# Kernel optimization log

Hardware: AMD Instinct MI355X
Metric: run time of the kernel (lower is better)

Reference implementation:

```python
import jax, jax.numpy as jnp
import numpy as np

B, NDOC, L, E = 32, 4, 512, 512
SCALE = np.float32(1.0 / np.sqrt(E))
NEG_INF = np.float32(-1e9)


def setup_inputs() -> dict:
    key = jax.random.key(0)
    k1, k2, k3, k4, k5, k6 = jax.random.split(key, 6)
    return {
        "x1": jax.random.normal(k1, (B, L, E), dtype=jnp.float32),
        "x2": jax.random.normal(k2, (B, NDOC, L, E), dtype=jnp.float32),
        "x1_len": jax.random.randint(k3, (B,), 0, L, dtype=jnp.int64),
        "x2_len": jax.random.randint(k4, (B, NDOC), 0, L, dtype=jnp.int64),
        "fusion_w": jax.random.normal(k5, (2 * E, E), dtype=jnp.float32) * 0.02,
        "fusion_b": jnp.zeros((E,), dtype=jnp.float32),
        "out_w": jax.random.normal(k6, (8 * E, 2 * E), dtype=jnp.float32) * 0.02,
        "out_b": jnp.zeros((2 * E,), dtype=jnp.float32),
    }


def reference(x1, x2, x1_len, x2_len, fusion_w, fusion_b, out_w, out_b):
    # Faithful to torch .repeat(1,4,...): concatenate 4 full copies along batch,
    # so attention row i pairs x1[i % B] with x2[i // 4, i % 4].
    x1_rep = jnp.tile(x1, (NDOC, 1, 1))          # [4B, L, E]
    x2_r = x2.reshape(-1, L, E)                  # [4B, L, E]

    x1_len_r = jnp.tile(x1_len, NDOC)            # [4B] (same tiling as x1_rep)
    x2_len_r = x2_len.reshape(-1)                # [4B]
    pos = jnp.arange(L)
    q_mask = pos[None, :] < x1_len_r[:, None]    # [4B, L]
    k_mask = pos[None, :] < x2_len_r[:, None]    # [4B, L]
    mask = q_mask[:, :, None] & k_mask[:, None, :]  # [4B, L, L]

    # scaled-dot-product attention with masked_fill(mask==0, -1e9)
    scores = jnp.einsum('bqe,bke->bqk', x1_rep, x2_r) * SCALE  # [4B, L, L]
    scores = jnp.where(mask, scores, NEG_INF)
    attn = jax.nn.softmax(scores, axis=-1)
    x1_att = jnp.einsum('bqk,bke->bqe', attn, x2_r)            # [4B, L, E]

    cat = jnp.concatenate([x1_rep - x1_att, x1_rep * x1_att], axis=-1)  # [4B, L, 2E]
    fus = jax.nn.relu(cat @ fusion_w + fusion_b)                        # [4B, L, E]

    x1_mean = jnp.mean(fus, axis=1)              # [4B, E]
    x1_max = jnp.max(fus, axis=1)                # [4B, E]
    pooled = jnp.concatenate([x1_mean.reshape(B, -1), x1_max.reshape(B, -1)], axis=-1)  # [B, 8E]
    out = jax.nn.relu(pooled @ out_w + out_b)    # [B, 2E]
    return out, attn
```

## Files before the change

kernel.cpp:

```cpp
#include <hip/hip_runtime.h>
#include <cstddef>

#define BATCH 32
#define NB    128
#define LL    512
#define EE    512
#define SCALE 0.044194173824159216f
#define NEG_INF -1e9f

typedef __attribute__((ext_vector_type(4))) float f32x4;
typedef __attribute__((ext_vector_type(8))) short s16x8;
typedef __attribute__((ext_vector_type(4))) unsigned short u16x4;

__device__ __forceinline__ unsigned short f2b(float f) {
    unsigned u = __float_as_uint(f);
    u += 0x7FFFu + ((u >> 16) & 1u);
    return (unsigned short)(u >> 16);
}
__device__ __forceinline__ float b2f(unsigned short h) {
    return __uint_as_float(((unsigned)h) << 16);
}

__global__ __launch_bounds__(256) void k_cvt_x1(
    const float* __restrict__ x1, unsigned short* __restrict__ x1bf)
{
    const size_t idx = (size_t)blockIdx.x * 256 + threadIdx.x;
    f32x4 v = *(const f32x4*)(x1 + idx * 4);
    u16x4 o = { f2b(v[0]), f2b(v[1]), f2b(v[2]), f2b(v[3]) };
    *(u16x4*)(x1bf + idx * 4) = o;
}

__global__ __launch_bounds__(256) void k_cvt_x2(
    const float* __restrict__ x2,
    unsigned short* __restrict__ x2bf, unsigned short* __restrict__ x2t)
{
    __shared__ float T[64][65];
    const int i = blockIdx.z, kb = blockIdx.y * 64, eb = blockIdx.x * 64;
    const float* src = x2 + (size_t)i * LL * EE;
    unsigned short* db = x2bf + (size_t)i * LL * EE;
    unsigned short* dt = x2t  + (size_t)i * LL * EE;
    const int t = threadIdx.x, r16 = t >> 4, c4 = (t & 15) * 4;
#pragma unroll
    for (int p = 0; p < 4; ++p) {
        int row = p * 16 + r16;
        f32x4 v = *(const f32x4*)(src + (size_t)(kb + row) * EE + eb + c4);
        T[row][c4] = v[0]; T[row][c4+1] = v[1]; T[row][c4+2] = v[2]; T[row][c4+3] = v[3];
        u16x4 o = { f2b(v[0]), f2b(v[1]), f2b(v[2]), f2b(v[3]) };
        *(u16x4*)(db + (size_t)(kb + row) * EE + eb + c4) = o;
    }
    __syncthreads();
#pragma unroll
    for (int p = 0; p < 4; ++p) {
        int erow = p * 16 + r16;
        u16x4 o = { f2b(T[c4][erow]), f2b(T[c4+1][erow]),
                    f2b(T[c4+2][erow]), f2b(T[c4+3][erow]) };
        *(u16x4*)(dt + (size_t)(eb + erow) * LL + kb + c4) = o;
    }
}

__global__ __launch_bounds__(256) void k_cvt_fw(
    const float* __restrict__ fw, unsigned short* __restrict__ fwt)
{
    __shared__ float T[64][65];
    const int jb = blockIdx.y * 64, eb = blockIdx.x * 64;
    const int t = threadIdx.x, r16 = t >> 4, c4 = (t & 15) * 4;
#pragma unroll
    for (int p = 0; p < 4; ++p) {
        int row = p * 16 + r16;
        f32x4 v = *(const f32x4*)(fw + (size_t)(jb + row) * EE + eb + c4);
        T[row][c4] = v[0]; T[row][c4+1] = v[1]; T[row][c4+2] = v[2]; T[row][c4+3] = v[3];
    }
    __syncthreads();
#pragma unroll
    for (int p = 0; p < 4; ++p) {
        int erow = p * 16 + r16;
        u16x4 o = { f2b(T[c4][erow]), f2b(T[c4+1][erow]),
                    f2b(T[c4+2][erow]), f2b(T[c4+3][erow]) };
        *(u16x4*)(fwt + (size_t)(eb + erow) * 1024 + jb + c4) = o;
    }
}

__global__ __launch_bounds__(256) void k_scores_mfma(
    const unsigned short* __restrict__ x1bf,
    const unsigned short* __restrict__ x2bf,
    const int* __restrict__ x1_len, const int* __restrict__ x2_len,
    float* __restrict__ attn)
{
    __shared__ unsigned short Al[128 * 40];
    __shared__ unsigned short Bl[128 * 40];
    const int i  = blockIdx.x;
    const int q0 = (blockIdx.y >> 2) * 128;
    const int k0 = (blockIdx.y & 3) * 128;
    const unsigned short* Ag = x1bf + (size_t)(i & 31) * LL * EE;
    const unsigned short* Bg = x2bf + (size_t)i * LL * EE;
    const int t = threadIdx.x, lane = t & 63;
    const int w = t >> 6, wrow = w >> 1, wcol = w & 1;
    const int m = lane & 15, quad = lane >> 4;
    const int srow = t >> 1, shalf = (t & 1) * 16;

    f32x4 acc[4][4];
#pragma unroll
    for (int r = 0; r < 4; ++r)
#pragma unroll
        for (int c = 0; c < 4; ++c) acc[r][c] = (f32x4){0.f, 0.f, 0.f, 0.f};

    for (int e0 = 0; e0 < EE; e0 += 32) {
        s16x8 a0 = *(const s16x8*)(Ag + (size_t)(q0 + srow) * EE + e0 + shalf);
        s16x8 a1 = *(const s16x8*)(Ag + (size_t)(q0 + srow) * EE + e0 + shalf + 8);
        s16x8 b0 = *(const s16x8*)(Bg + (size_t)(k0 + srow) * EE + e0 + shalf);
        s16x8 b1 = *(const s16x8*)(Bg + (size_t)(k0 + srow) * EE + e0 + shalf + 8);
        __syncthreads();
        *(s16x8*)&Al[srow * 40 + shalf]     = a0;
        *(s16x8*)&Al[srow * 40 + shalf + 8] = a1;
        *(s16x8*)&Bl[srow * 40 + shalf]     = b0;
        *(s16x8*)&Bl[srow * 40 + shalf + 8] = b1;
        __syncthreads();
        s16x8 af[4], bfr[4];
#pragma unroll
        for (int rt = 0; rt < 4; ++rt)
            af[rt] = *(const s16x8*)&Al[(wrow * 64 + rt * 16 + m) * 40 + quad * 8];
#pragma unroll
        for (int ct = 0; ct < 4; ++ct)
            bfr[ct] = *(const s16x8*)&Bl[(wcol * 64 + ct * 16 + m) * 40 + quad * 8];
#pragma unroll
        for (int rt = 0; rt < 4; ++rt)
#pragma unroll
            for (int ct = 0; ct < 4; ++ct)
                acc[rt][ct] = __builtin_amdgcn_mfma_f32_16x16x32_bf16(
                    af[rt], bfr[ct], acc[rt][ct], 0, 0, 0);
    }

    const int qlen = x1_len[i & 31];
    const int klen = x2_len[i];
    float* op = attn + (size_t)i * LL * LL;
#pragma unroll
    for (int rt = 0; rt < 4; ++rt) {
#pragma unroll
        for (int reg = 0; reg < 4; ++reg) {
            const int q = q0 + wrow * 64 + rt * 16 + quad * 4 + reg;
            const bool qok = q < qlen;
#pragma unroll
            for (int ct = 0; ct < 4; ++ct) {
                const int k = k0 + wcol * 64 + ct * 16 + m;
                float v = (qok && k < klen) ? acc[rt][ct][reg] * SCALE : NEG_INF;
                op[(size_t)q * LL + k] = v;
            }
        }
    }
}

__global__ __launch_bounds__(256) void k_softmax(
    float* __restrict__ attn, unsigned short* __restrict__ attnbf)
{
    const int row  = blockIdx.x * 4 + (threadIdx.x >> 6);
    const int lane = threadIdx.x & 63;
    float* p = attn + (size_t)row * LL + lane * 8;
    float4 v0 = *(float4*)p;
    float4 v1 = *(float4*)(p + 4);
    float mx = fmaxf(fmaxf(fmaxf(v0.x, v0.y), fmaxf(v0.z, v0.w)),
                     fmaxf(fmaxf(v1.x, v1.y), fmaxf(v1.z, v1.w)));
#pragma unroll
    for (int o = 32; o > 0; o >>= 1) mx = fmaxf(mx, __shfl_xor(mx, o));
    v0.x = __expf(v0.x - mx); v0.y = __expf(v0.y - mx);
    v0.z = __expf(v0.z - mx); v0.w = __expf(v0.w - mx);
    v1.x = __expf(v1.x - mx); v1.y = __expf(v1.y - mx);
    v1.z = __expf(v1.z - mx); v1.w = __expf(v1.w - mx);
    float s = v0.x + v0.y + v0.z + v0.w + v1.x + v1.y + v1.z + v1.w;
#pragma unroll
    for (int o = 32; o > 0; o >>= 1) s += __shfl_xor(s, o);
    const float inv = 1.0f / s;
    v0.x *= inv; v0.y *= inv; v0.z *= inv; v0.w *= inv;
    v1.x *= inv; v1.y *= inv; v1.z *= inv; v1.w *= inv;
    *(float4*)p = v0;
    *(float4*)(p + 4) = v1;
    unsigned short* pb = attnbf + (size_t)row * LL + lane * 8;
    u16x4 o0 = { f2b(v0.x), f2b(v0.y), f2b(v0.z), f2b(v0.w) };
    u16x4 o1 = { f2b(v1.x), f2b(v1.y), f2b(v1.z), f2b(v1.w) };
    *(u16x4*)pb       = o0;
    *(u16x4*)(pb + 4) = o1;
}

__global__ __launch_bounds__(256) void k_pv_mfma(
    const unsigned short* __restrict__ attnbf,
    const unsigned short* __restrict__ x2t,
    const unsigned short* __restrict__ x1bf,
    unsigned short* __restrict__ Cbuf)
{
    __shared__ unsigned short Al[128 * 40];
    __shared__ unsigned short Bl[128 * 40];
    const int i  = blockIdx.x;
    const int q0 = (blockIdx.y >> 2) * 128;
    const int e0 = (blockIdx.y & 3) * 128;
    const unsigned short* Ag = attnbf + (size_t)i * LL * LL;
    const unsigned short* Bg = x2t   + (size_t)i * LL * EE;
    const int t = threadIdx.x, lane = t & 63;
    const int w = t >> 6, wrow = w >> 1, wcol = w & 1;
    const int m = lane & 15, quad = lane >> 4;
    const int srow = t >> 1, shalf = (t & 1) * 16;

    f32x4 acc[4][4];
#pragma unroll
    for (int r = 0; r < 4; ++r)
#pragma unroll
        for (int c = 0; c < 4; ++c) acc[r][c] = (f32x4){0.f, 0.f, 0.f, 0.f};

    for (int kk0 = 0; kk0 < LL; kk0 += 32) {
        s16x8 a0 = *(const s16x8*)(Ag + (size_t)(q0 + srow) * LL + kk0 + shalf);
        s16x8 a1 = *(const s16x8*)(Ag + (size_t)(q0 + srow) * LL + kk0 + shalf + 8);
        s16x8 b0 = *(const s16x8*)(Bg + (size_t)(e0 + srow) * LL + kk0 + shalf);
        s16x8 b1 = *(const s16x8*)(Bg + (size_t)(e0 + srow) * LL + kk0 + shalf + 8);
        __syncthreads();
        *(s16x8*)&Al[srow * 40 + shalf]     = a0;
        *(s16x8*)&Al[srow * 40 + shalf + 8] = a1;
        *(s16x8*)&Bl[srow * 40 + shalf]     = b0;
        *(s16x8*)&Bl[srow * 40 + shalf + 8] = b1;
        __syncthreads();
        s16x8 af[4], bfr[4];
#pragma unroll
        for (int rt = 0; rt < 4; ++rt)
            af[rt] = *(const s16x8*)&Al[(wrow * 64 + rt * 16 + m) * 40 + quad * 8];
#pragma unroll
        for (int ct = 0; ct < 4; ++ct)
            bfr[ct] = *(const s16x8*)&Bl[(wcol * 64 + ct * 16 + m) * 40 + quad * 8];
#pragma unroll
        for (int rt = 0; rt < 4; ++rt)
#pragma unroll
            for (int ct = 0; ct < 4; ++ct)
                acc[rt][ct] = __builtin_amdgcn_mfma_f32_16x16x32_bf16(
                    af[rt], bfr[ct], acc[rt][ct], 0, 0, 0);
    }

    const unsigned short* x1p = x1bf + (size_t)(i & 31) * LL * EE;
    unsigned short* Cb = Cbuf + (size_t)i * LL * 1024;
#pragma unroll
    for (int rt = 0; rt < 4; ++rt) {
#pragma unroll
        for (int reg = 0; reg < 4; ++reg) {
            const int l = q0 + wrow * 64 + rt * 16 + quad * 4 + reg;
#pragma unroll
            for (int ct = 0; ct < 4; ++ct) {
                const int e = e0 + wcol * 64 + ct * 16 + m;
                float att = acc[rt][ct][reg];
                float xv  = b2f(x1p[(size_t)l * EE + e]);
                Cb[(size_t)l * 1024 + e]       = f2b(xv - att);
                Cb[(size_t)l * 1024 + 512 + e] = f2b(xv * att);
            }
        }
    }
}

__global__ __launch_bounds__(256) void k_fuse_mfma(
    const unsigned short* __restrict__ Cbuf,
    const unsigned short* __restrict__ fwt,
    const float* __restrict__ fb,
    float* __restrict__ pmean, float* __restrict__ pmax)
{
    __shared__ unsigned short Al[128 * 40];
    __shared__ unsigned short Bl[128 * 40];
    __shared__ float psum[2][128];
    __shared__ float pmx[2][128];
    const int i  = blockIdx.x;
    const int lt = blockIdx.y >> 2;
    const int e0 = (blockIdx.y & 3) * 128;
    const unsigned short* Ab = Cbuf + ((size_t)i * LL + lt * 128) * 1024;
    const int t = threadIdx.x, lane = t & 63;
    const int w = t >> 6, wrow = w >> 1, wcol = w & 1;
    const int m = lane & 15, quad = lane >> 4;
    const int srow = t >> 1, shalf = (t & 1) * 16;

    float bias[4];
#pragma unroll
    for (int ct = 0; ct < 4; ++ct) bias[ct] = fb[e0 + wcol * 64 + ct * 16 + m];
    float csum[4] = {0.f, 0.f, 0.f, 0.f};
    float cmax[4] = {-3e38f, -3e38f, -3e38f, -3e38f};

    f32x4 acc[4][4];
#pragma unroll
    for (int r = 0; r < 4; ++r)
#pragma unroll
        for (int c = 0; c < 4; ++c) acc[r][c] = (f32x4){0.f, 0.f, 0.f, 0.f};

    for (int j0 = 0; j0 < 1024; j0 += 32) {
        s16x8 a0 = *(const s16x8*)(Ab + (size_t)srow * 1024 + j0 + shalf);
        s16x8 a1 = *(const s16x8*)(Ab + (size_t)srow * 1024 + j0 + shalf + 8);
        s16x8 b0 = *(const s16x8*)(fwt + (size_t)(e0 + srow) * 1024 + j0 + shalf);
        s16x8 b1 = *(const s16x8*)(fwt + (size_t)(e0 + srow) * 1024 + j0 + shalf + 8);
        __syncthreads();
        *(s16x8*)&Al[srow * 40 + shalf]     = a0;
        *(s16x8*)&Al[srow * 40 + shalf + 8] = a1;
        *(s16x8*)&Bl[srow * 40 + shalf]     = b0;
        *(s16x8*)&Bl[srow * 40 + shalf + 8] = b1;
        __syncthreads();
        s16x8 af[4], bfr[4];
#pragma unroll
        for (int rt = 0; rt < 4; ++rt)
            af[rt] = *(const s16x8*)&Al[(wrow * 64 + rt * 16 + m) * 40 + quad * 8];
#pragma unroll
        for (int ct = 0; ct < 4; ++ct)
            bfr[ct] = *(const s16x8*)&Bl[(wcol * 64 + ct * 16 + m) * 40 + quad * 8];
#pragma unroll
        for (int rt = 0; rt < 4; ++rt)
#pragma unroll
            for (int ct = 0; ct < 4; ++ct)
                acc[rt][ct] = __builtin_amdgcn_mfma_f32_16x16x32_bf16(
                    af[rt], bfr[ct], acc[rt][ct], 0, 0, 0);
    }
#pragma unroll
    for (int rt = 0; rt < 4; ++rt)
#pragma unroll
        for (int reg = 0; reg < 4; ++reg)
#pragma unroll
            for (int ct = 0; ct < 4; ++ct) {
                float f = fmaxf(acc[rt][ct][reg] + bias[ct], 0.f);
                csum[ct] += f;
                cmax[ct] = fmaxf(cmax[ct], f);
            }
#pragma unroll
    for (int ct = 0; ct < 4; ++ct) {
        csum[ct] += __shfl_xor(csum[ct], 16);
        csum[ct] += __shfl_xor(csum[ct], 32);
        cmax[ct] = fmaxf(cmax[ct], __shfl_xor(cmax[ct], 16));
        cmax[ct] = fmaxf(cmax[ct], __shfl_xor(cmax[ct], 32));
    }
    if (quad == 0) {
#pragma unroll
        for (int ct = 0; ct < 4; ++ct) {
            psum[wrow][wcol * 64 + ct * 16 + m] = csum[ct];
            pmx[wrow][wcol * 64 + ct * 16 + m] = cmax[ct];
        }
    }
    __syncthreads();
    if (t < 128) {
        float s  = psum[0][t] + psum[1][t];
        float mx = fmaxf(pmx[0][t], pmx[1][t]);
        pmean[((size_t)i * 4 + lt) * EE + e0 + t] = s;
        pmax[((size_t)i * 4 + lt) * EE + e0 + t]  = mx;
    }
}

__global__ __launch_bounds__(256) void k_out_split(
    const float* __restrict__ pmean, const float* __restrict__ pmax,
    const float* __restrict__ ow, float* __restrict__ partial)
{
    __shared__ float ps[256];
    const int kc = blockIdx.x;
    const int b  = blockIdx.y;
    const int t  = threadIdx.x;
    const int j  = kc * 256 + t;
    const int jj = (j < 2048) ? j : j - 2048;
    const int ii = 4 * b + (jj >> 9);
    const int e  = jj & 511;
    float v;
    if (j < 2048) {
        const float* bp = pmean + (size_t)ii * 4 * EE + e;
        v = (bp[0] + bp[512] + bp[1024] + bp[1536]) * (1.0f / 512.0f);
    } else {
        const float* bp = pmax + (size_t)ii * 4 * EE + e;
        v = fmaxf(fmaxf(bp[0], bp[512]), fmaxf(bp[1024], bp[1536]));
    }
    ps[t] = v;
    __syncthreads();
    f32x4 acc = {0.f, 0.f, 0.f, 0.f};
    const float* wp = ow + (size_t)kc * 256 * 1024 + t * 4;
#pragma unroll 8
    for (int q = 0; q < 256; ++q) {
        f32x4 w4 = *(const f32x4*)(wp + (size_t)q * 1024);
        float p = ps[q];
        acc[0] = fmaf(p, w4[0], acc[0]);
        acc[1] = fmaf(p, w4[1], acc[1]);
        acc[2] = fmaf(p, w4[2], acc[2]);
        acc[3] = fmaf(p, w4[3], acc[3]);
    }
    *(f32x4*)(partial + ((size_t)kc * 32 + b) * 1024 + t * 4) = acc;
}

__global__ __launch_bounds__(256) void k_out_final(
    const float* __restrict__ partial, const float* __restrict__ ob,
    float* __restrict__ out)
{
    const int idx = blockIdx.x * 256 + threadIdx.x;
    const int b = idx >> 10, o = idx & 1023;
    float s = ob[o];
#pragma unroll
    for (int kc = 0; kc < 16; ++kc)
        s += partial[((size_t)kc * 32 + b) * 1024 + o];
    out[idx] = fmaxf(s, 0.f);
}

extern "C" void kernel_launch(void* const* d_in, const int* in_sizes, int n_in,
                              void* d_out, int out_size, void* d_ws, size_t ws_size,
                              hipStream_t stream)
{
    const float* x1     = (const float*)d_in[0];
    const float* x2     = (const float*)d_in[1];
    const int*   x1_len = (const int*)d_in[2];
    const int*   x2_len = (const int*)d_in[3];
    const float* fw     = (const float*)d_in[4];
    const float* fb     = (const float*)d_in[5];
    const float* ow     = (const float*)d_in[6];
    const float* ob     = (const float*)d_in[7];

    float* out  = (float*)d_out;
    float* attn = out + (size_t)BATCH * 1024;

    char* wp = (char*)d_ws;
    unsigned short* x1bf   = (unsigned short*)wp; wp += (size_t)BATCH * LL * EE * 2;
    unsigned short* x2bf   = (unsigned short*)wp; wp += (size_t)NB * LL * EE * 2;
    unsigned short* x2t    = (unsigned short*)wp; wp += (size_t)NB * LL * EE * 2;
    unsigned short* attnbf = (unsigned short*)wp; wp += (size_t)NB * LL * LL * 2;
    unsigned short* Cbuf   = (unsigned short*)wp; wp += (size_t)NB * LL * 1024 * 2;
    unsigned short* fwt    = (unsigned short*)wp; wp += (size_t)EE * 1024 * 2;
    float* pmean   = (float*)wp; wp += (size_t)NB * 4 * EE * 4;
    float* pmax    = (float*)wp; wp += (size_t)NB * 4 * EE * 4;
    float* partial = (float*)wp; wp += (size_t)16 * BATCH * 1024 * 4;

    k_cvt_x1<<<dim3(BATCH * LL * EE / 4 / 256), 256, 0, stream>>>(x1, x1bf);
    k_cvt_x2<<<dim3(8, 8, NB), 256, 0, stream>>>(x2, x2bf, x2t);
    k_cvt_fw<<<dim3(8, 16), 256, 0, stream>>>(fw, fwt);
    k_scores_mfma<<<dim3(128, 16), 256, 0, stream>>>(x1bf, x2bf, x1_len, x2_len, attn);
    k_softmax<<<dim3(NB * LL / 4), 256, 0, stream>>>(attn, attnbf);
    k_pv_mfma<<<dim3(128, 16), 256, 0, stream>>>(attnbf, x2t, x1bf, Cbuf);
    k_fuse_mfma<<<dim3(128, 16), 256, 0, stream>>>(Cbuf, fwt, fb, pmean, pmax);
    k_out_split<<<dim3(16, BATCH), 256, 0, stream>>>(pmean, pmax, ow, partial);
    k_out_final<<<dim3(BATCH * 1024 / 256), 256, 0, stream>>>(partial, ob, out);
}
```

Measured before the change: 659.2 us.

## Load GEMM tiles directly into LDS and interleave concat buffer columns

Each of the three bf16 MFMA GEMM kernels now stages tiles with global_load_lds (direct global-to-LDS, 16 bytes per lane) instead of loading into registers and writing to LDS. The LDS row stride drops from padded 40 to unpadded 32, and the barrier moves to after the MFMAs. Separately, the concat buffer now stores the (x-att, x*att) pair as one interleaved 32-bit write, and the fusion weight transpose is permuted to match. The aim is to cut register staging and the VGPR round trip, and to halve the store count in the PV epilogue. The risks are more LDS bank conflicts on the unpadded fragment reads and slower scattered 2-byte writes in the weight conversion.

```diff
diff --git a/kernel.cpp b/kernel.cpp
--- a/kernel.cpp
+++ b/kernel.cpp
@@ -21,6 +21,12 @@
     return __uint_as_float(((unsigned)h) << 16);
 }
 
+__device__ __forceinline__ void gld_lds16(const unsigned short* g, unsigned short* l) {
+    __builtin_amdgcn_global_load_lds(
+        (const __attribute__((address_space(1))) void*)g,
+        (__attribute__((address_space(3))) void*)l, 16, 0, 0);
+}
+
 __global__ __launch_bounds__(256) void k_cvt_x1(
     const float* __restrict__ x1, unsigned short* __restrict__ x1bf)
 {
@@ -74,9 +80,12 @@
 #pragma unroll
     for (int p = 0; p < 4; ++p) {
         int erow = p * 16 + r16;
-        u16x4 o = { f2b(T[c4][erow]), f2b(T[c4+1][erow]),
-                    f2b(T[c4+2][erow]), f2b(T[c4+3][erow]) };
-        *(u16x4*)(fwt + (size_t)(eb + erow) * 1024 + jb + c4) = o;
+#pragma unroll
+        for (int k = 0; k < 4; ++k) {
+            int jold = jb + c4 + k;
+            int jn = (jold < 512) ? (2 * jold) : (2 * (jold - 512) + 1);
+            fwt[(size_t)(eb + erow) * 1024 + jn] = f2b(T[c4 + k][erow]);
+        }
     }
 }
 
@@ -86,8 +95,8 @@
     const int* __restrict__ x1_len, const int* __restrict__ x2_len,
     float* __restrict__ attn)
 {
-    __shared__ unsigned short Al[128 * 40];
-    __shared__ unsigned short Bl[128 * 40];
+    __shared__ unsigned short Al[128 * 32];
+    __shared__ unsigned short Bl[128 * 32];
     const int i  = blockIdx.x;
     const int q0 = (blockIdx.y >> 2) * 128;
     const int k0 = (blockIdx.y & 3) * 128;
@@ -96,7 +105,7 @@
     const int t = threadIdx.x, lane = t & 63;
     const int w = t >> 6, wrow = w >> 1, wcol = w & 1;
     const int m = lane & 15, quad = lane >> 4;
-    const int srow = t >> 1, shalf = (t & 1) * 16;
+    const int lrow = lane >> 2, lcol = (lane & 3) * 8;
 
     f32x4 acc[4][4];
 #pragma unroll
@@ -105,29 +114,27 @@
         for (int c = 0; c < 4; ++c) acc[r][c] = (f32x4){0.f, 0.f, 0.f, 0.f};
 
     for (int e0 = 0; e0 < EE; e0 += 32) {
-        s16x8 a0 = *(const s16x8*)(Ag + (size_t)(q0 + srow) * EE + e0 + shalf);
-        s16x8 a1 = *(const s16x8*)(Ag + (size_t)(q0 + srow) * EE + e0 + shalf + 8);
-        s16x8 b0 = *(const s16x8*)(Bg + (size_t)(k0 + srow) * EE + e0 + shalf);
-        s16x8 b1 = *(const s16x8*)(Bg + (size_t)(k0 + srow) * EE + e0 + shalf + 8);
-        __syncthreads();
-        *(s16x8*)&Al[srow * 40 + shalf]     = a0;
-        *(s16x8*)&Al[srow * 40 + shalf + 8] = a1;
-        *(s16x8*)&Bl[srow * 40 + shalf]     = b0;
-        *(s16x8*)&Bl[srow * 40 + shalf + 8] = b1;
+#pragma unroll
+        for (int c = 0; c < 2; ++c) {
+            const int s = c * 4 + w;
+            gld_lds16(Ag + (size_t)(q0 + s * 16 + lrow) * EE + e0 + lcol, &Al[s * 512]);
+            gld_lds16(Bg + (size_t)(k0 + s * 16 + lrow) * EE + e0 + lcol, &Bl[s * 512]);
+        }
         __syncthreads();
         s16x8 af[4], bfr[4];
 #pragma unroll
         for (int rt = 0; rt < 4; ++rt)
-            af[rt] = *(const s16x8*)&Al[(wrow * 64 + rt * 16 + m) * 40 + quad * 8];
+            af[rt] = *(const s16x8*)&Al[(wrow * 64 + rt * 16 + m) * 32 + quad * 8];
 #pragma unroll
         for (int ct = 0; ct < 4; ++ct)
-            bfr[ct] = *(const s16x8*)&Bl[(wcol * 64 + ct * 16 + m) * 40 + quad * 8];
+            bfr[ct] = *(const s16x8*)&Bl[(wcol * 64 + ct * 16 + m) * 32 + quad * 8];
 #pragma unroll
         for (int rt = 0; rt < 4; ++rt)
 #pragma unroll
             for (int ct = 0; ct < 4; ++ct)
                 acc[rt][ct] = __builtin_amdgcn_mfma_f32_16x16x32_bf16(
                     af[rt], bfr[ct], acc[rt][ct], 0, 0, 0);
+        __syncthreads();
     }
 
     const int qlen = x1_len[i & 31];
@@ -186,8 +193,8 @@
     const unsigned short* __restrict__ x1bf,
     unsigned short* __restrict__ Cbuf)
 {
-    __shared__ unsigned short Al[128 * 40];
-    __shared__ unsigned short Bl[128 * 40];
+    __shared__ unsigned short Al[128 * 32];
+    __shared__ unsigned short Bl[128 * 32];
     const int i  = blockIdx.x;
     const int q0 = (blockIdx.y >> 2) * 128;
     const int e0 = (blockIdx.y & 3) * 128;
@@ -196,7 +203,7 @@
     const int t = threadIdx.x, lane = t & 63;
     const int w = t >> 6, wrow = w >> 1, wcol = w & 1;
     const int m = lane & 15, quad = lane >> 4;
-    const int srow = t >> 1, shalf = (t & 1) * 16;
+    const int lrow = lane >> 2, lcol = (lane & 3) * 8;
 
     f32x4 acc[4][4];
 #pragma unroll
@@ -205,29 +212,27 @@
         for (int c = 0; c < 4; ++c) acc[r][c] = (f32x4){0.f, 0.f, 0.f, 0.f};
 
     for (int kk0 = 0; kk0 < LL; kk0 += 32) {
-        s16x8 a0 = *(const s16x8*)(Ag + (size_t)(q0 + srow) * LL + kk0 + shalf);
-        s16x8 a1 = *(const s16x8*)(Ag + (size_t)(q0 + srow) * LL + kk0 + shalf + 8);
-        s16x8 b0 = *(const s16x8*)(Bg + (size_t)(e0 + srow) * LL + kk0 + shalf);
-        s16x8 b1 = *(const s16x8*)(Bg + (size_t)(e0 + srow) * LL + kk0 + shalf + 8);
-        __syncthreads();
-        *(s16x8*)&Al[srow * 40 + shalf]     = a0;
-        *(s16x8*)&Al[srow * 40 + shalf + 8] = a1;
-        *(s16x8*)&Bl[srow * 40 + shalf]     = b0;
-        *(s16x8*)&Bl[srow * 40 + shalf + 8] = b1;
+#pragma unroll
+        for (int c = 0; c < 2; ++c) {
+            const int s = c * 4 + w;
+            gld_lds16(Ag + (size_t)(q0 + s * 16 + lrow) * LL + kk0 + lcol, &Al[s * 512]);
+            gld_lds16(Bg + (size_t)(e0 + s * 16 + lrow) * LL + kk0 + lcol, &Bl[s * 512]);
+        }
         __syncthreads();
         s16x8 af[4], bfr[4];
 #pragma unroll
         for (int rt = 0; rt < 4; ++rt)
-            af[rt] = *(const s16x8*)&Al[(wrow * 64 + rt * 16 + m) * 40 + quad * 8];
+            af[rt] = *(const s16x8*)&Al[(wrow * 64 + rt * 16 + m) * 32 + quad * 8];
 #pragma unroll
         for (int ct = 0; ct < 4; ++ct)
-            bfr[ct] = *(const s16x8*)&Bl[(wcol * 64 + ct * 16 + m) * 40 + quad * 8];
+            bfr[ct] = *(const s16x8*)&Bl[(wcol * 64 + ct * 16 + m) * 32 + quad * 8];
 #pragma unroll
         for (int rt = 0; rt < 4; ++rt)
 #pragma unroll
             for (int ct = 0; ct < 4; ++ct)
                 acc[rt][ct] = __builtin_amdgcn_mfma_f32_16x16x32_bf16(
                     af[rt], bfr[ct], acc[rt][ct], 0, 0, 0);
+        __syncthreads();
     }
 
     const unsigned short* x1p = x1bf + (size_t)(i & 31) * LL * EE;
@@ -242,8 +247,8 @@
                 const int e = e0 + wcol * 64 + ct * 16 + m;
                 float att = acc[rt][ct][reg];
                 float xv  = b2f(x1p[(size_t)l * EE + e]);
-                Cb[(size_t)l * 1024 + e]       = f2b(xv - att);
-                Cb[(size_t)l * 1024 + 512 + e] = f2b(xv * att);
+                unsigned pr = (unsigned)f2b(xv - att) | ((unsigned)f2b(xv * att) << 16);
+                *(unsigned*)(Cb + (size_t)l * 1024 + 2 * e) = pr;
             }
         }
     }
@@ -255,8 +260,8 @@
     const float* __restrict__ fb,
     float* __restrict__ pmean, float* __restrict__ pmax)
 {
-    __shared__ unsigned short Al[128 * 40];
-    __shared__ unsigned short Bl[128 * 40];
+    __shared__ unsigned short Al[128 * 32];
+    __shared__ unsigned short Bl[128 * 32];
     __shared__ float psum[2][128];
     __shared__ float pmx[2][128];
     const int i  = blockIdx.x;
@@ -266,7 +271,7 @@
     const int t = threadIdx.x, lane = t & 63;
     const int w = t >> 6, wrow = w >> 1, wcol = w & 1;
     const int m = lane & 15, quad = lane >> 4;
-    const int srow = t >> 1, shalf = (t & 1) * 16;
+    const int lrow = lane >> 2, lcol = (lane & 3) * 8;
 
     float bias[4];
 #pragma unroll
@@ -281,29 +286,27 @@
         for (int c = 0; c < 4; ++c) acc[r][c] = (f32x4){0.f, 0.f, 0.f, 0.f};
 
     for (int j0 = 0; j0 < 1024; j0 += 32) {
-        s16x8 a0 = *(const s16x8*)(Ab + (size_t)srow * 1024 + j0 + shalf);
-        s16x8 a1 = *(const s16x8*)(Ab + (size_t)srow * 1024 + j0 + shalf + 8);
-        s16x8 b0 = *(const s16x8*)(fwt + (size_t)(e0 + srow) * 1024 + j0 + shalf);
-        s16x8 b1 = *(const s16x8*)(fwt + (size_t)(e0 + srow) * 1024 + j0 + shalf + 8);
-        __syncthreads();
-        *(s16x8*)&Al[srow * 40 + shalf]     = a0;
-        *(s16x8*)&Al[srow * 40 + shalf + 8] = a1;
-        *(s16x8*)&Bl[srow * 40 + shalf]     = b0;
-        *(s16x8*)&Bl[srow * 40 + shalf + 8] = b1;
+#pragma unroll
+        for (int c = 0; c < 2; ++c) {
+            const int s = c * 4 + w;
+            gld_lds16(Ab + (size_t)(s * 16 + lrow) * 1024 + j0 + lcol, &Al[s * 512]);
+            gld_lds16(fwt + (size_t)(e0 + s * 16 + lrow) * 1024 + j0 + lcol, &Bl[s * 512]);
+        }
         __syncthreads();
         s16x8 af[4], bfr[4];
 #pragma unroll
         for (int rt = 0; rt < 4; ++rt)
-            af[rt] = *(const s16x8*)&Al[(wrow * 64 + rt * 16 + m) * 40 + quad * 8];
+            af[rt] = *(const s16x8*)&Al[(wrow * 64 + rt * 16 + m) * 32 + quad * 8];
 #pragma unroll
         for (int ct = 0; ct < 4; ++ct)
-            bfr[ct] = *(const s16x8*)&Bl[(wcol * 64 + ct * 16 + m) * 40 + quad * 8];
+            bfr[ct] = *(const s16x8*)&Bl[(wcol * 64 + ct * 16 + m) * 32 + quad * 8];
 #pragma unroll
         for (int rt = 0; rt < 4; ++rt)
 #pragma unroll
             for (int ct = 0; ct < 4; ++ct)
                 acc[rt][ct] = __builtin_amdgcn_mfma_f32_16x16x32_bf16(
                     af[rt], bfr[ct], acc[rt][ct], 0, 0, 0);
+        __syncthreads();
     }
 #pragma unroll
     for (int rt = 0; rt < 4; ++rt)
```

Result: faster. 637.0 us (-3.4%).
